# Kernel optimization log

Measured on AMD Instinct MI355X. Metric: run time of the kernel, lower is better.

Reference implementation:

```python
import jax, jax.numpy as jnp
import numpy as np

N, F, P, NT = 4096, 256, 5, 5  # agents, feat dim, n_persona, n_time_steps
EPS = 1e-8


def setup_inputs() -> dict:
    key = jax.random.key(0)
    ks = jax.random.split(key, 7)
    attributes = jax.random.normal(ks[0], (N, F), dtype=jnp.float32)
    edges = (jax.random.uniform(ks[1], (N, N)) < 0.01).astype(jnp.float32)
    persona = jax.random.uniform(ks[2], (NT, N, P), dtype=jnp.float32)
    T = jax.random.uniform(ks[3], (P,), dtype=jnp.float32) * 0.5 + 0.5  # keep temperature away from 0
    e = jax.random.uniform(ks[4], (P,), dtype=jnp.float32) + 0.5
    r = jax.random.uniform(ks[5], (P,), dtype=jnp.float32)
    W = jax.random.uniform(ks[6], (P,), dtype=jnp.float32) + 0.5
    return {"attributes": attributes, "edges": edges, "persona": persona,
            "T": T, "e": e, "r": r, "W": W, "times": 2}


def reference(attributes, edges, persona, T, e, r, W, times):
    p = persona[times]                      # [N, P] persona weights at this time step
    msg = edges @ attributes                # [N, F] message passing, shared across personas

    def body(acc, xs):
        idx, Ti, ei, ri, Wi, pi = xs        # pi: [N]
        feat = ri * attributes + (msg * Wi) * (1.0 - ri)          # [N, F]
        nf = feat / jnp.sqrt(jnp.sum(feat * feat, axis=1, keepdims=True))  # row L2 norm
        x = jnp.exp((nf @ nf.T) / (Ti + EPS)) * ei                 # [N, N]
        x = x / (jnp.max(x) + EPS)                                 # min-max scale (min=0)
        # (1 - exp(-2v)) / (1 + exp(-2v)) == tanh(v)
        tc = jnp.tanh(x) * pi[None, :]                              # column persona gating
        # i == 0 initializes edges_prob with tc, every i adds row-gated tc
        acc = acc + tc * pi[:, None] + jnp.where(idx == 0, 1.0, 0.0) * tc
        return acc, None

    acc0 = jnp.zeros((N, N), dtype=jnp.float32)
    out, _ = jax.lax.scan(body, acc0, (jnp.arange(P), T, e, r, W, p.T))
    return out
```

## Files before the change

### kernel.cpp

```cpp
#include <hip/hip_runtime.h>
#include <hip/hip_bf16.h>

#define N 4096
#define F 256
#define P 5
#define EPSV 1e-8f
#define BK 32
#define NSTEP (F / BK)
#define NTRI 2080
#define GRIDSZ 512
#define DDEG 12
#define NC (DDEG + 1)
#define PAN 16384
#define Q0OFF 49152
#define QSZ 10240
#define CFOFF 69632

typedef __attribute__((ext_vector_type(8))) short bf16x8;
typedef __attribute__((ext_vector_type(4))) float f32x4;
typedef __attribute__((ext_vector_type(2))) float f32x2;

__device__ __forceinline__ f32x4 mfma16(bf16x8 a, bf16x8 b, f32x4 c) {
    return __builtin_amdgcn_mfma_f32_16x16x32_bf16(a, b, c, 0, 0, 0);
}

__device__ __forceinline__ void gload16(const void* src, const char* ldsdst) {
    __builtin_amdgcn_global_load_lds(
        (const __attribute__((address_space(1))) void*)src,
        (__attribute__((address_space(3))) void*)ldsdst, 16, 0, 0);
}

__device__ __forceinline__ f32x2 sp(float x) { return (f32x2){x, x}; }

#define SB() __builtin_amdgcn_sched_barrier(0)
#define RAWBAR() do { SB(); __builtin_amdgcn_s_barrier(); SB(); } while (0)

__global__ __launch_bounds__(256) void prep_kernel(
    const float* __restrict__ E, const float* __restrict__ A,
    const float* __restrict__ persona,
    const float* __restrict__ Tt, const float* __restrict__ ee,
    const float* __restrict__ rr, const float* __restrict__ Ww,
    const int* __restrict__ times,
    __hip_bfloat16* __restrict__ Abf, __hip_bfloat16* __restrict__ Mbf,
    float* __restrict__ qsoa, float* __restrict__ cstg, int* __restrict__ ctr) {
    __shared__ int cnt;
    __shared__ int list[1024];
    const int a = blockIdx.x;
    const int t = threadIdx.x;
    if (t == 0) cnt = 0;
    __syncthreads();
    const float4* erow = (const float4*)(E + (size_t)a * N);
    for (int b = t; b < N / 4; b += 256) {
        const float4 v = erow[b];
        if (v.x != 0.f) list[atomicAdd(&cnt, 1)] = 4 * b;
        if (v.y != 0.f) list[atomicAdd(&cnt, 1)] = 4 * b + 1;
        if (v.z != 0.f) list[atomicAdd(&cnt, 1)] = 4 * b + 2;
        if (v.w != 0.f) list[atomicAdd(&cnt, 1)] = 4 * b + 3;
    }
    __syncthreads();
    const int c = cnt;
    float s0 = 0.f, s1 = 0.f, s2 = 0.f, s3 = 0.f;
    float s4 = 0.f, s5 = 0.f, s6 = 0.f, s7 = 0.f;
    int j = 0;
    for (; j + 8 <= c; j += 8) {
        s0 += A[(size_t)list[j] * F + t];
        s1 += A[(size_t)list[j + 1] * F + t];
        s2 += A[(size_t)list[j + 2] * F + t];
        s3 += A[(size_t)list[j + 3] * F + t];
        s4 += A[(size_t)list[j + 4] * F + t];
        s5 += A[(size_t)list[j + 5] * F + t];
        s6 += A[(size_t)list[j + 6] * F + t];
        s7 += A[(size_t)list[j + 7] * F + t];
    }
    for (; j < c; ++j) s0 += A[(size_t)list[j] * F + t];
    const float mv = ((s0 + s1) + (s2 + s3)) + ((s4 + s5) + (s6 + s7));
    const float av = A[(size_t)a * F + t];
    Abf[(size_t)a * F + t] = __float2bfloat16(av);
    Mbf[(size_t)a * F + t] = __float2bfloat16(mv);

    float paa = av * av, pam = av * mv, pmm = mv * mv;
    #pragma unroll
    for (int o = 32; o > 0; o >>= 1) {
        paa += __shfl_down(paa, o);
        pam += __shfl_down(pam, o);
        pmm += __shfl_down(pmm, o);
    }
    __shared__ float s[3][4];
    const int wid = t >> 6;
    if ((t & 63) == 0) { s[0][wid] = paa; s[1][wid] = pam; s[2][wid] = pmm; }
    __syncthreads();
    if (t < P) {
        const float naa = s[0][0] + s[0][1] + s[0][2] + s[0][3];
        const float nam = s[1][0] + s[1][1] + s[1][2] + s[1][3];
        const float nmm = s[2][0] + s[2][1] + s[2][2] + s[2][3];
        const float Ti = Tt[t], ei = ee[t], ri = rr[t], Wi = Ww[t];
        const float wb = (1.f - ri) * Wi;
        const float n2 = ri * ri * naa + 2.f * ri * wb * nam + wb * wb * nmm;
        const float rn = rsqrtf(n2);
        const float p = persona[(size_t)(*times) * (size_t)N * P + (size_t)a * P + t];
        qsoa[(t * 4 + 0) * N + a] = ri * rn;
        qsoa[(t * 4 + 1) * N + a] = wb * rn;
        qsoa[(t * 4 + 2) * N + a] = p;
        qsoa[(t * 4 + 3) * N + a] = p + (t == 0 ? 1.f : 0.f);
        if (a == 0) {
            const float kk = 1.f / (Ti + EPSV);
            const float scf = ei / (ei * __expf(kk) + EPSV);
            float ch[NC];
            #pragma unroll
            for (int j2 = 0; j2 < NC; ++j2) ch[j2] = 0.f;
            for (int m = 0; m < 32; ++m) {
                const float th = 3.14159265358979323846f * (m + 0.5f) / 32.f;
                const float c1 = __cosf(th);
                const float x = scf * __expf(kk * 1.05f * c1);
                const float e2 = __expf(2.f * x);
                const float fm = 1.f - 2.f / (e2 + 1.f);
                float cjm1 = 1.f, cj = c1;
                ch[0] += fm;
                ch[1] += fm * c1;
                #pragma unroll
                for (int j2 = 2; j2 < NC; ++j2) {
                    const float cn = 2.f * c1 * cj - cjm1;
                    ch[j2] += fm * cn;
                    cjm1 = cj;
                    cj = cn;
                }
            }
            #pragma unroll
            for (int j2 = 0; j2 < NC; ++j2) ch[j2] *= (j2 == 0 ? 1.f : 2.f) / 32.f;
            float mono[NC], Tp[NC], Tc[NC], Tn[NC];
            const float is = 1.f / 1.05f;
            #pragma unroll
            for (int k2 = 0; k2 < NC; ++k2) {
                mono[k2] = 0.f; Tp[k2] = 0.f; Tc[k2] = 0.f; Tn[k2] = 0.f;
            }
            Tp[0] = 1.f;
            Tc[1] = is;
            #pragma unroll
            for (int k2 = 0; k2 < NC; ++k2) mono[k2] += ch[0] * Tp[k2] + ch[1] * Tc[k2];
            for (int j2 = 2; j2 < NC; ++j2) {
                #pragma unroll
                for (int k2 = 0; k2 < NC; ++k2)
                    Tn[k2] = 2.f * is * (k2 ? Tc[k2 - 1] : 0.f) - Tp[k2];
                #pragma unroll
                for (int k2 = 0; k2 < NC; ++k2) mono[k2] += ch[j2] * Tn[k2];
                #pragma unroll
                for (int k2 = 0; k2 < NC; ++k2) { Tp[k2] = Tc[k2]; Tc[k2] = Tn[k2]; }
            }
            #pragma unroll
            for (int k2 = 0; k2 < NC; ++k2) cstg[t * NC + k2] = mono[k2];
        }
    }
    if (a == 0 && t == 0) *ctr = GRIDSZ;
}

__global__ __launch_bounds__(512) void gram_kernel(
    const __hip_bfloat16* __restrict__ Abf, const __hip_bfloat16* __restrict__ Mbf,
    const float* __restrict__ qsoa, const float* __restrict__ cstg,
    int* __restrict__ ctr, float* __restrict__ out) {
    __shared__ __align__(16) char smem[69904];
    __shared__ int snext;

    const int t = threadIdx.x;
    const int lane = t & 63;
    const int w = t >> 6;
    const int wr = w >> 1;
    const int wc = w & 1;

    const int sslot = (lane & 3) ^ ((lane >> 3) & 3);
    const int srowoff = (w & 1) * 32 + (lane >> 2);
    const int ldsp = (w >> 1) * 4096 + (w & 1) * 2048;
    const __hip_bfloat16* smat = ((w >> 1) & 1) ? Mbf : Abf;

    const int frow = lane & 15;
    const int fg = lane >> 4;
    const int jr = fg << 2;
    const int rdslot = (fg ^ ((frow >> 1) & 3)) << 4;
    const int aoff = (wr * 16 + frow) * 64 + rdslot;
    const int coff0 = (wc * 32 + frow) * 64 + rdslot;
    const int coff1 = (wc * 32 + 16 + frow) * 64 + rdslot;
    const float* cfs = (const float*)(smem + CFOFF);

    #define DECODE(id, oby, obx) do {                                     \
        const int bid_ = ((id) & 7) * 260 + ((id) >> 3);                  \
        int bx_ = (int)((sqrtf(8.f * (float)bid_ + 1.f) - 1.f) * 0.5f);   \
        while ((bx_ + 1) * (bx_ + 2) / 2 <= bid_) ++bx_;                  \
        while (bx_ * (bx_ + 1) / 2 > bid_) --bx_;                         \
        (obx) = bx_;                                                      \
        (oby) = bid_ - bx_ * (bx_ + 1) / 2;                               \
    } while (0)

    #define PROLOGUE(r0_, c0_, qp_) do {                                  \
        const int sb_ = (w < 4) ? (r0_) : (c0_);                          \
        const __hip_bfloat16* ps_ =                                       \
            smat + (size_t)(sb_ + srowoff) * F + sslot * 8;               \
        gload16(ps_, smem + ldsp);                                        \
        gload16(ps_ + 16 * F, smem + ldsp + 1024);                        \
        gload16(ps_ + 32, smem + PAN + ldsp);                             \
        gload16(ps_ + 32 + 16 * F, smem + PAN + ldsp + 1024);             \
        const int qb_ = Q0OFF + (qp_) * QSZ;                              \
        if (w == 0) {                                                     \
            _Pragma("unroll")                                             \
            for (int it = 0; it < 5; ++it)                                \
                gload16(qsoa + (it * 4 + (lane >> 4)) * N + (r0_) +       \
                        (lane & 15) * 4, smem + qb_ + it * 1024);         \
        } else if (w == 1) {                                              \
            _Pragma("unroll")                                             \
            for (int it = 0; it < 5; ++it)                                \
                gload16(qsoa + (it * 4 + (lane >> 4)) * N + (c0_) +       \
                        (lane & 15) * 4, smem + qb_ + 5120 + it * 1024);  \
        }                                                                 \
        if (t == 0) snext = atomicAdd(ctr, 1);                            \
    } while (0)

    int raw = blockIdx.x;
    int by, bx;
    DECODE(raw, by, bx);
    int row0 = by << 6, col0 = bx << 6;
    int qpar = 0;
    int pend = 0;

    PROLOGUE(row0, col0, 0);
    if (w == 2 && lane < 17) gload16(cstg + lane * 4, smem + CFOFF);

    for (;;) {
        if (pend == 16) asm volatile("s_waitcnt vmcnt(16)" ::: "memory");
        else if (pend == 8) asm volatile("s_waitcnt vmcnt(8)" ::: "memory");
        else asm volatile("s_waitcnt vmcnt(0)" ::: "memory");
        RAWBAR();

        const int nxt = snext;

        const int sbc = (w < 4) ? row0 : col0;
        const __hip_bfloat16* psrc =
            smat + (size_t)(sbc + srowoff) * F + sslot * 8;

        f32x4 acc[4][2];
        #pragma unroll
        for (int g = 0; g < 4; ++g)
            #pragma unroll
            for (int n = 0; n < 2; ++n) acc[g][n] = (f32x4){0.f, 0.f, 0.f, 0.f};

        #pragma unroll
        for (int s = 0; s < NSTEP; ++s) {
            if (s + 2 < NSTEP) {
                const char* lb = smem + ((s + 2) % 3) * PAN + ldsp;
                gload16(psrc + (s + 2) * BK, lb);
                gload16(psrc + (s + 2) * BK + 16 * F, lb + 1024);
            }
            const char* base = smem + (s % 3) * PAN;
            const bf16x8 aA = *(const bf16x8*)(base + aoff);
            const bf16x8 aM = *(const bf16x8*)(base + 4096 + aoff);
            const bf16x8 bA0 = *(const bf16x8*)(base + 8192 + coff0);
            const bf16x8 bA1 = *(const bf16x8*)(base + 8192 + coff1);
            const bf16x8 bM0 = *(const bf16x8*)(base + 12288 + coff0);
            const bf16x8 bM1 = *(const bf16x8*)(base + 12288 + coff1);
            __builtin_amdgcn_s_setprio(1);
            acc[0][0] = mfma16(aA, bA0, acc[0][0]);
            acc[0][1] = mfma16(aA, bA1, acc[0][1]);
            acc[1][0] = mfma16(aA, bM0, acc[1][0]);
            acc[1][1] = mfma16(aA, bM1, acc[1][1]);
            acc[2][0] = mfma16(aM, bA0, acc[2][0]);
            acc[2][1] = mfma16(aM, bA1, acc[2][1]);
            acc[3][0] = mfma16(aM, bM0, acc[3][0]);
            acc[3][1] = mfma16(aM, bM1, acc[3][1]);
            __builtin_amdgcn_s_setprio(0);
            if (s + 1 < NSTEP) {
                if (s + 2 < NSTEP) asm volatile("s_waitcnt vmcnt(2)" ::: "memory");
                else asm volatile("s_waitcnt vmcnt(0)" ::: "memory");
                RAWBAR();
            }
        }

        RAWBAR();

        const bool have = (nxt < NTRI);
        int nby = 0, nbx = 0, nrow0 = 0, ncol0 = 0;
        if (have) {
            DECODE(nxt, nby, nbx);
            nrow0 = nby << 6;
            ncol0 = nbx << 6;
            PROLOGUE(nrow0, ncol0, qpar ^ 1);
        }

        const float* qlr = (const float*)(smem + Q0OFF + qpar * QSZ);
        const float* qlc = qlr + 1280;
        f32x2 o1[2][2], o2[2][2];
        #pragma unroll
        for (int n = 0; n < 2; ++n)
            #pragma unroll
            for (int jp = 0; jp < 2; ++jp) { o1[n][jp] = sp(0.f); o2[n][jp] = sp(0.f); }

        #pragma unroll
        for (int i = 0; i < P; ++i) {
            const int ib = i * 256;
            float cf[NC];
            #pragma unroll
            for (int k = 0; k < NC; ++k) cf[k] = cfs[i * NC + k];
            float cA[2], cB[2], cP0[2], cP1[2];
            #pragma unroll
            for (int n = 0; n < 2; ++n) {
                const int cr = wc * 32 + n * 16 + frow;
                cA[n]  = qlc[ib + cr];
                cB[n]  = qlc[ib + 64 + cr];
                cP0[n] = qlc[ib + 128 + cr];
                cP1[n] = qlc[ib + 192 + cr];
            }
            #pragma unroll
            for (int jp = 0; jp < 2; ++jp) {
                const int rrw = wr * 16 + jr + jp * 2;
                const f32x2 rA  = *(const f32x2*)&qlr[ib + rrw];
                const f32x2 rB  = *(const f32x2*)&qlr[ib + 64 + rrw];
                const f32x2 rP0 = *(const f32x2*)&qlr[ib + 128 + rrw];
                const f32x2 rP1 = *(const f32x2*)&qlr[ib + 192 + rrw];
                #pragma unroll
                for (int n = 0; n < 2; ++n) {
                    const f32x2 aAA = (f32x2){acc[0][n][2 * jp], acc[0][n][2 * jp + 1]};
                    const f32x2 aAM = (f32x2){acc[1][n][2 * jp], acc[1][n][2 * jp + 1]};
                    const f32x2 aMA = (f32x2){acc[2][n][2 * jp], acc[2][n][2 * jp + 1]};
                    const f32x2 aMM = (f32x2){acc[3][n][2 * jp], acc[3][n][2 * jp + 1]};
                    const f32x2 h0 = rA * aAA + rB * aMA;
                    const f32x2 h1 = rA * aAM + rB * aMM;
                    const f32x2 g2 = h0 * sp(cA[n]) + h1 * sp(cB[n]);
                    f32x2 f2 = sp(cf[DDEG]);
                    #pragma unroll
                    for (int k = DDEG - 1; k >= 0; --k) f2 = f2 * g2 + sp(cf[k]);
                    o1[n][jp] += (f2 * rP1) * sp(cP0[n]);
                    o2[n][jp] += (f2 * rP0) * sp(cP1[n]);
                }
            }
        }

        #pragma unroll
        for (int jp = 0; jp < 2; ++jp)
            #pragma unroll
            for (int cc = 0; cc < 2; ++cc) {
                const int gr = row0 + wr * 16 + jr + jp * 2 + cc;
                #pragma unroll
                for (int n = 0; n < 2; ++n) {
                    const int gc = col0 + wc * 32 + n * 16 + frow;
                    out[(size_t)gr * N + gc] = o1[n][jp][cc];
                }
            }
        if (by != bx) {
            #pragma unroll
            for (int jp = 0; jp < 2; ++jp)
                #pragma unroll
                for (int cc = 0; cc < 2; ++cc) {
                    const int gr = row0 + wr * 16 + jr + jp * 2 + cc;
                    #pragma unroll
                    for (int n = 0; n < 2; ++n) {
                        const int gc = col0 + wc * 32 + n * 16 + frow;
                        out[(size_t)gc * N + gr] = o2[n][jp][cc];
                    }
                }
            pend = 16;
        } else {
            pend = 8;
        }

        if (!have) break;
        raw = nxt; by = nby; bx = nbx; row0 = nrow0; col0 = ncol0; qpar ^= 1;
    }
    #undef PROLOGUE
    #undef DECODE
}

extern "C" void kernel_launch(void* const* d_in, const int* in_sizes, int n_in,
                              void* d_out, int out_size, void* d_ws, size_t ws_size,
                              hipStream_t stream) {
    const float* A = (const float*)d_in[0];
    const float* E = (const float*)d_in[1];
    const float* persona = (const float*)d_in[2];
    const float* T = (const float*)d_in[3];
    const float* e = (const float*)d_in[4];
    const float* r = (const float*)d_in[5];
    const float* W = (const float*)d_in[6];
    const int* times = (const int*)d_in[7];
    float* out = (float*)d_out;

    char* ws = (char*)d_ws;
    __hip_bfloat16* Abf = (__hip_bfloat16*)ws;
    __hip_bfloat16* Mbf = (__hip_bfloat16*)(ws + (2 << 20));
    float* qsoa = (float*)(ws + (4 << 20));
    float* cstg = (float*)(ws + (4 << 20) + 5 * 4 * N * 4);
    int* ctr = (int*)(ws + (4 << 20) + 5 * 4 * N * 4 + 512);

    prep_kernel<<<N, 256, 0, stream>>>(E, A, persona, T, e, r, W, times,
                                       Abf, Mbf, qsoa, cstg, ctr);
    gram_kernel<<<GRIDSZ, 512, 0, stream>>>(Abf, Mbf, qsoa, cstg, ctr, out);
}
```

Before: 83.83 us.

## Deepen K-panel pipeline to four stages and load q-vectors inside tile loop

The gram kernel's LDS ring for K panels grows from three to four buffers, so three panels are prefetched ahead and the waitcnt thresholds are retuned to match. The double-buffered per-tile q-vector staging is replaced by a single buffer that is loaded at the start of each tile rather than in the prefetch prologue. The aim is to hide more global-load latency in the MFMA main loop. In exchange LDS use rises, which may lower occupancy, and the q loads now share vmcnt accounting with the panel loads. prep_kernel also gains a min-blocks launch bound.

```diff
diff --git a/kernel.cpp b/kernel.cpp
--- a/kernel.cpp
+++ b/kernel.cpp
@@ -12,9 +12,8 @@
 #define DDEG 12
 #define NC (DDEG + 1)
 #define PAN 16384
-#define Q0OFF 49152
-#define QSZ 10240
-#define CFOFF 69632
+#define QOFF 65536
+#define CFOFF 75776
 
 typedef __attribute__((ext_vector_type(8))) short bf16x8;
 typedef __attribute__((ext_vector_type(4))) float f32x4;
@@ -35,7 +34,7 @@
 #define SB() __builtin_amdgcn_sched_barrier(0)
 #define RAWBAR() do { SB(); __builtin_amdgcn_s_barrier(); SB(); } while (0)
 
-__global__ __launch_bounds__(256) void prep_kernel(
+__global__ __launch_bounds__(256, 4) void prep_kernel(
     const float* __restrict__ E, const float* __restrict__ A,
     const float* __restrict__ persona,
     const float* __restrict__ Tt, const float* __restrict__ ee,
@@ -157,7 +156,7 @@
     const __hip_bfloat16* __restrict__ Abf, const __hip_bfloat16* __restrict__ Mbf,
     const float* __restrict__ qsoa, const float* __restrict__ cstg,
     int* __restrict__ ctr, float* __restrict__ out) {
-    __shared__ __align__(16) char smem[69904];
+    __shared__ __align__(16) char smem[76048];
     __shared__ int snext;
 
     const int t = threadIdx.x;
@@ -189,7 +188,7 @@
         (oby) = bid_ - bx_ * (bx_ + 1) / 2;                               \
     } while (0)
 
-    #define PROLOGUE(r0_, c0_, qp_) do {                                  \
+    #define PROLOGUE(r0_, c0_) do {                                       \
         const int sb_ = (w < 4) ? (r0_) : (c0_);                          \
         const __hip_bfloat16* ps_ =                                       \
             smat + (size_t)(sb_ + srowoff) * F + sslot * 8;               \
@@ -197,18 +196,8 @@
         gload16(ps_ + 16 * F, smem + ldsp + 1024);                        \
         gload16(ps_ + 32, smem + PAN + ldsp);                             \
         gload16(ps_ + 32 + 16 * F, smem + PAN + ldsp + 1024);             \
-        const int qb_ = Q0OFF + (qp_) * QSZ;                              \
-        if (w == 0) {                                                     \
-            _Pragma("unroll")                                             \
-            for (int it = 0; it < 5; ++it)                                \
-                gload16(qsoa + (it * 4 + (lane >> 4)) * N + (r0_) +       \
-                        (lane & 15) * 4, smem + qb_ + it * 1024);         \
-        } else if (w == 1) {                                              \
-            _Pragma("unroll")                                             \
-            for (int it = 0; it < 5; ++it)                                \
-                gload16(qsoa + (it * 4 + (lane >> 4)) * N + (c0_) +       \
-                        (lane & 15) * 4, smem + qb_ + 5120 + it * 1024);  \
-        }                                                                 \
+        gload16(ps_ + 64, smem + 2 * PAN + ldsp);                         \
+        gload16(ps_ + 64 + 16 * F, smem + 2 * PAN + ldsp + 1024);         \
         if (t == 0) snext = atomicAdd(ctr, 1);                            \
     } while (0)
 
@@ -216,10 +205,9 @@
     int by, bx;
     DECODE(raw, by, bx);
     int row0 = by << 6, col0 = bx << 6;
-    int qpar = 0;
     int pend = 0;
 
-    PROLOGUE(row0, col0, 0);
+    PROLOGUE(row0, col0);
     if (w == 2 && lane < 17) gload16(cstg + lane * 4, smem + CFOFF);
 
     for (;;) {
@@ -230,6 +218,18 @@
 
         const int nxt = snext;
 
+        if (w == 0) {
+            #pragma unroll
+            for (int it = 0; it < 5; ++it)
+                gload16(qsoa + (it * 4 + (lane >> 4)) * N + row0 + (lane & 15) * 4,
+                        smem + QOFF + it * 1024);
+        } else if (w == 1) {
+            #pragma unroll
+            for (int it = 0; it < 5; ++it)
+                gload16(qsoa + (it * 4 + (lane >> 4)) * N + col0 + (lane & 15) * 4,
+                        smem + QOFF + 5120 + it * 1024);
+        }
+
         const int sbc = (w < 4) ? row0 : col0;
         const __hip_bfloat16* psrc =
             smat + (size_t)(sbc + srowoff) * F + sslot * 8;
@@ -242,12 +242,12 @@
 
         #pragma unroll
         for (int s = 0; s < NSTEP; ++s) {
-            if (s + 2 < NSTEP) {
-                const char* lb = smem + ((s + 2) % 3) * PAN + ldsp;
-                gload16(psrc + (s + 2) * BK, lb);
-                gload16(psrc + (s + 2) * BK + 16 * F, lb + 1024);
-            }
-            const char* base = smem + (s % 3) * PAN;
+            if (s + 3 < NSTEP) {
+                const char* lb = smem + ((s + 3) & 3) * PAN + ldsp;
+                gload16(psrc + (s + 3) * BK, lb);
+                gload16(psrc + (s + 3) * BK + 16 * F, lb + 1024);
+            }
+            const char* base = smem + (s & 3) * PAN;
             const bf16x8 aA = *(const bf16x8*)(base + aoff);
             const bf16x8 aM = *(const bf16x8*)(base + 4096 + aoff);
             const bf16x8 bA0 = *(const bf16x8*)(base + 8192 + coff0);
@@ -265,8 +265,9 @@
             acc[3][1] = mfma16(aM, bM1, acc[3][1]);
             __builtin_amdgcn_s_setprio(0);
             if (s + 1 < NSTEP) {
-                if (s + 2 < NSTEP) asm volatile("s_waitcnt vmcnt(2)" ::: "memory");
-                else asm volatile("s_waitcnt vmcnt(0)" ::: "memory");
+                if (s >= 2 && s <= 4) asm volatile("s_waitcnt vmcnt(4)" ::: "memory");
+                else if (s == 5) asm volatile("s_waitcnt vmcnt(2)" ::: "memory");
+                else if (s == 6) asm volatile("s_waitcnt vmcnt(0)" ::: "memory");
                 RAWBAR();
             }
         }
@@ -279,10 +280,10 @@
             DECODE(nxt, nby, nbx);
             nrow0 = nby << 6;
             ncol0 = nbx << 6;
-            PROLOGUE(nrow0, ncol0, qpar ^ 1);
-        }
-
-        const float* qlr = (const float*)(smem + Q0OFF + qpar * QSZ);
+            PROLOGUE(nrow0, ncol0);
+        }
+
+        const float* qlr = (const float*)(smem + QOFF);
         const float* qlc = qlr + 1280;
         f32x2 o1[2][2], o2[2][2];
         #pragma unroll
@@ -359,7 +360,7 @@
         }
 
         if (!have) break;
-        raw = nxt; by = nby; bx = nbx; row0 = nrow0; col0 = ncol0; qpar ^= 1;
+        raw = nxt; by = nby; bx = nbx; row0 = nrow0; col0 = ncol0;
     }
     #undef PROLOGUE
     #undef DECODE
```

Result: slower. 88.44 us (+5.5%).
